# Kernel optimization log

Hardware: AMD Instinct MI355X
Metric: run time of the kernel (lower is better)

Reference implementation:

```python
import jax, jax.numpy as jnp
import numpy as np

N_NODES = 100000
F_IN = 64
F_OUT = 64
SLOPE = 0.2


def setup_inputs() -> dict:
    key = jax.random.key(0)
    k1, k2, k3, k4 = jax.random.split(key, 4)
    input_matrix = jax.random.normal(k1, (N_NODES, F_IN), dtype=jnp.float32)
    edge_index = jax.random.randint(k2, (2, 1600000), 0, N_NODES, dtype=jnp.int64)
    # xavier-uniform-style params
    lim_w = float(np.sqrt(6.0 / (F_IN + F_OUT)))
    W = jax.random.uniform(k3, (F_IN, F_OUT), minval=-lim_w, maxval=lim_w, dtype=jnp.float32)
    lim_a = float(np.sqrt(6.0 / (2 * F_OUT + 1)))
    a = jax.random.uniform(k4, (2 * F_OUT,), minval=-lim_a, maxval=lim_a, dtype=jnp.float32)
    return {"input_matrix": input_matrix, "edge_index": edge_index, "W": W, "a": a}


def reference(input_matrix, edge_index, W, a):
    N = input_matrix.shape[0]
    # add self edges
    loops = jnp.arange(N, dtype=edge_index.dtype)
    src = jnp.concatenate([edge_index[0], loops])  # [E+N]
    dst = jnp.concatenate([edge_index[1], loops])  # [E+N]

    h = input_matrix @ W                      # [N, F_out]
    F = h.shape[1]
    h_src = h[src]                            # [E+N, F_out] gather
    h_dst = h[dst]                            # [E+N, F_out] gather
    # cat([h_src, h_dst], 1) @ a == h_src @ a[:F] + h_dst @ a[F:]
    alpha = h_src @ a[:F] + h_dst @ a[F:]     # [E+N]
    alpha = jnp.where(alpha >= 0, alpha, SLOPE * alpha)  # leaky relu
    alpha = jnp.exp(alpha)
    denom = jax.ops.segment_sum(alpha, src, num_segments=N)  # [N]
    alpha = alpha / denom[src]                # segment softmax over edges sharing src
    out = jax.ops.segment_sum(h_dst * alpha[:, None], src, num_segments=N)  # [N, F_out]
    return out
```

## Files before the change

### kernel.cpp

```cpp
#include <hip/hip_runtime.h>
#include <hip/hip_bf16.h>

#define F 64
#define SLOPE 0.2f
#define NB_SHIFT 8
#define BATCH 4096
#define SLAB 5120

typedef __attribute__((ext_vector_type(8))) short bf16x8;
typedef __attribute__((ext_vector_type(4))) float f32x4;

__device__ inline unsigned short f2bf(float f) {
    unsigned u = __float_as_uint(f);
    unsigned r = (u + 0x7FFFu + ((u >> 16) & 1u)) >> 16;
    return (unsigned short)r;
}

__global__ __launch_bounds__(256) void gat_prep(
    const float* __restrict__ W, const float* __restrict__ a,
    unsigned short* __restrict__ Wp, float* __restrict__ w1,
    float* __restrict__ w2, int* __restrict__ bucketCursor) {
    int tid = threadIdx.x;
    for (int i = tid; i < 512; i += 256) bucketCursor[i] = i * SLAB;

    if (tid < 64) {
#pragma unroll
        for (int f = 0; f < 8; ++f) {
            int cg = f >> 1, kc = f & 1;
            int col = cg * 16 + (tid & 15);
            unsigned short us[8];
#pragma unroll
            for (int j = 0; j < 8; ++j) {
                int k = kc * 32 + (tid >> 4) * 8 + j;
                us[j] = f2bf(W[k * F + col]);
            }
            uint4 pk;
            pk.x = us[0] | ((unsigned)us[1] << 16);
            pk.y = us[2] | ((unsigned)us[3] << 16);
            pk.z = us[4] | ((unsigned)us[5] << 16);
            pk.w = us[6] | ((unsigned)us[7] << 16);
            *(uint4*)&Wp[(f * 64 + tid) * 8] = pk;
        }
    } else if (tid < 128) {
        int k = tid - 64;
        float acc1 = 0.f, acc2 = 0.f;
#pragma unroll
        for (int n = 0; n < F; ++n) {
            float wv = W[k * F + n];
            acc1 = fmaf(wv, a[n], acc1);
            acc2 = fmaf(wv, a[F + n], acc2);
        }
        w1[k] = acc1;
        w2[k] = acc2;
    }
}

__global__ __launch_bounds__(512) void gat_gemm_bin(
    const float* __restrict__ X, const unsigned short* __restrict__ Wp,
    const float* __restrict__ w1, const float* __restrict__ w2,
    unsigned short* __restrict__ hb, float* __restrict__ s1,
    float* __restrict__ s2, int N,
    const int* __restrict__ src, const int* __restrict__ dst,
    int* __restrict__ bucketCursor, unsigned* __restrict__ bucketData, int E,
    int gemmBlocks) {
    __shared__ int hist[512], excl[512], gbase[512], cur[512];
    __shared__ int wsum[8];
    __shared__ int2 staged[BATCH];

    int tid = threadIdx.x;
    int lane = tid & 63, wid = tid >> 6;

    if ((int)blockIdx.x >= gemmBlocks) {
        int base = (blockIdx.x - gemmBlocks) * BATCH;
        int n = E - base;
        if (n > BATCH) n = BATCH;

        hist[tid] = 0;
        __syncthreads();

        int se[8], de[8];
#pragma unroll
        for (int j = 0; j < 8; ++j) {
            int i = base + j * 512 + tid;
            se[j] = -1;
            de[j] = 0;
            if (i < E) {
                se[j] = src[i];
                de[j] = dst[i];
                atomicAdd(&hist[se[j] >> NB_SHIFT], 1);
            }
        }
        __syncthreads();
        int v = hist[tid];
        int x = v;
#pragma unroll
        for (int off = 1; off < 64; off <<= 1) {
            int y = __shfl_up(x, off, 64);
            if (lane >= off) x += y;
        }
        if (lane == 63) wsum[wid] = x;
        __syncthreads();
        int add = 0;
        for (int w = 0; w < 8; ++w)
            if (w < wid) add += wsum[w];
        int ex = add + x - v;
        excl[tid] = ex;
        cur[tid] = ex;
        __syncthreads();
#pragma unroll
        for (int j = 0; j < 8; ++j) {
            if (se[j] >= 0) {
                int b = se[j] >> NB_SHIFT;
                int pos = atomicAdd(&cur[b], 1);
                staged[pos] = make_int2(se[j], de[j]);
            }
        }
        if (v > 0)
            gbase[tid] = atomicAdd(&bucketCursor[tid], v);
        __syncthreads();
        for (int i = tid; i < n; i += 512) {
            int2 p = staged[i];
            int b = p.x >> NB_SHIFT;
            bucketData[gbase[b] + (i - excl[b])] =
                ((unsigned)(p.x & 255) << 24) | (unsigned)p.y;
        }
        return;
    }

    int rowBase = blockIdx.x * 128 + wid * 16;
    if (rowBase >= N) return;
    int lrow = lane & 15;
    int kg = lane >> 4;
    int row = rowBase + lrow;
    int rclamp = (row < N) ? row : (N - 1);

    const float* xp = &X[(size_t)rclamp * F + kg * 8];
    float4 u0 = *(const float4*)(xp + 0);
    float4 u1 = *(const float4*)(xp + 4);
    float4 u2 = *(const float4*)(xp + 32);
    float4 u3 = *(const float4*)(xp + 36);
    float xr[16] = {u0.x, u0.y, u0.z, u0.w, u1.x, u1.y, u1.z, u1.w,
                    u2.x, u2.y, u2.z, u2.w, u3.x, u3.y, u3.z, u3.w};

    bf16x8 a0, a1;
#pragma unroll
    for (int j = 0; j < 8; ++j) {
        a0[j] = (short)f2bf(xr[j]);
        a1[j] = (short)f2bf(xr[8 + j]);
    }

    bf16x8 bf0 = *(const bf16x8*)&Wp[(0 * 64 + lane) * 8];
    bf16x8 bf1 = *(const bf16x8*)&Wp[(1 * 64 + lane) * 8];
    bf16x8 bf2 = *(const bf16x8*)&Wp[(2 * 64 + lane) * 8];
    bf16x8 bf3 = *(const bf16x8*)&Wp[(3 * 64 + lane) * 8];
    bf16x8 bf4 = *(const bf16x8*)&Wp[(4 * 64 + lane) * 8];
    bf16x8 bf5 = *(const bf16x8*)&Wp[(5 * 64 + lane) * 8];
    bf16x8 bf6 = *(const bf16x8*)&Wp[(6 * 64 + lane) * 8];
    bf16x8 bf7 = *(const bf16x8*)&Wp[(7 * 64 + lane) * 8];

    f32x4 acc0 = {0.f, 0.f, 0.f, 0.f};
    f32x4 acc1v = {0.f, 0.f, 0.f, 0.f};
    f32x4 acc2v = {0.f, 0.f, 0.f, 0.f};
    f32x4 acc3 = {0.f, 0.f, 0.f, 0.f};
    acc0 = __builtin_amdgcn_mfma_f32_16x16x32_bf16(a0, bf0, acc0, 0, 0, 0);
    acc0 = __builtin_amdgcn_mfma_f32_16x16x32_bf16(a1, bf1, acc0, 0, 0, 0);
    acc1v = __builtin_amdgcn_mfma_f32_16x16x32_bf16(a0, bf2, acc1v, 0, 0, 0);
    acc1v = __builtin_amdgcn_mfma_f32_16x16x32_bf16(a1, bf3, acc1v, 0, 0, 0);
    acc2v = __builtin_amdgcn_mfma_f32_16x16x32_bf16(a0, bf4, acc2v, 0, 0, 0);
    acc2v = __builtin_amdgcn_mfma_f32_16x16x32_bf16(a1, bf5, acc2v, 0, 0, 0);
    acc3 = __builtin_amdgcn_mfma_f32_16x16x32_bf16(a0, bf6, acc3, 0, 0, 0);
    acc3 = __builtin_amdgcn_mfma_f32_16x16x32_bf16(a1, bf7, acc3, 0, 0, 0);

#pragma unroll
    for (int r = 0; r < 4; ++r) {
        int ro = rowBase + kg * 4 + r;
        if (ro < N) {
            size_t rb = (size_t)ro * F + lrow;
            hb[rb + 0] = f2bf(acc0[r]);
            hb[rb + 16] = f2bf(acc1v[r]);
            hb[rb + 32] = f2bf(acc2v[r]);
            hb[rb + 48] = f2bf(acc3[r]);
        }
    }

    float4 wa0 = *(const float4*)&w1[kg * 8];
    float4 wa1 = *(const float4*)&w1[kg * 8 + 4];
    float4 wa2 = *(const float4*)&w1[32 + kg * 8];
    float4 wa3 = *(const float4*)&w1[32 + kg * 8 + 4];
    float4 wb0 = *(const float4*)&w2[kg * 8];
    float4 wb1 = *(const float4*)&w2[kg * 8 + 4];
    float4 wb2 = *(const float4*)&w2[32 + kg * 8];
    float4 wb3 = *(const float4*)&w2[32 + kg * 8 + 4];
    float wv1[16] = {wa0.x, wa0.y, wa0.z, wa0.w, wa1.x, wa1.y, wa1.z, wa1.w,
                     wa2.x, wa2.y, wa2.z, wa2.w, wa3.x, wa3.y, wa3.z, wa3.w};
    float wv2[16] = {wb0.x, wb0.y, wb0.z, wb0.w, wb1.x, wb1.y, wb1.z, wb1.w,
                     wb2.x, wb2.y, wb2.z, wb2.w, wb3.x, wb3.y, wb3.z, wb3.w};
    float p = 0.f, q = 0.f;
#pragma unroll
    for (int j = 0; j < 16; ++j) {
        p = fmaf(xr[j], wv1[j], p);
        q = fmaf(xr[j], wv2[j], q);
    }
    p += __shfl_xor(p, 16, 64);
    p += __shfl_xor(p, 32, 64);
    q += __shfl_xor(q, 16, 64);
    q += __shfl_xor(q, 32, 64);
    if (lane < 16 && row < N) {
        s1[row] = p;
        s2[row] = q;
    }
}

__global__ __launch_bounds__(256) void gat_bucket(
    const int* __restrict__ bucketCursor, const unsigned* __restrict__ bucketData,
    const float* __restrict__ s1, const float* __restrict__ s2,
    int* __restrict__ rowbeg, int* __restrict__ rowend,
    int2* __restrict__ sortedData, int N) {
    __shared__ int cnt[256], cur[256];
    __shared__ float s1l[256];
    __shared__ int wsum[4];
    int b = blockIdx.x;
    int tid = threadIdx.x, lane = tid & 63, wid = tid >> 6;
    int beg = b * SLAB;
    int end = bucketCursor[b];
    int node0 = b << NB_SHIFT;
    int node = node0 + tid;

    cnt[tid] = 0;
    s1l[tid] = (node < N) ? s1[node] : 0.f;
    __syncthreads();
    for (int i = beg + tid; i < end; i += 256)
        atomicAdd(&cnt[bucketData[i] >> 24], 1);
    __syncthreads();
    int v = cnt[tid];
    int x = v;
#pragma unroll
    for (int off = 1; off < 64; off <<= 1) {
        int y = __shfl_up(x, off, 64);
        if (lane >= off) x += y;
    }
    if (lane == 63) wsum[wid] = x;
    __syncthreads();
    int add = 0;
    for (int w = 0; w < 4; ++w)
        if (w < wid) add += wsum[w];
    int excl = add + x - v;
    if (node < N) {
        rowbeg[node] = beg + excl;
        rowend[node] = beg + excl + v;
    }
    cur[tid] = beg + excl;
    __syncthreads();
    for (int i = beg + tid; i < end; i += 256) {
        unsigned w = bucketData[i];
        int sloc = w >> 24;
        int d = (int)(w & 0xFFFFFFu);
        float t = s1l[sloc] + s2[d];
        t = (t >= 0.f) ? t : SLOPE * t;
        float al = expf(t);
        int pos = atomicAdd(&cur[sloc], 1);
        sortedData[pos] = make_int2(d, __float_as_int(al));
    }
}

#define EDGE_FMA(g, al, A)                                                   \
    A[0] = fmaf(al, __uint_as_float(g.x << 16), A[0]);                       \
    A[1] = fmaf(al, __uint_as_float(g.x & 0xFFFF0000u), A[1]);               \
    A[2] = fmaf(al, __uint_as_float(g.y << 16), A[2]);                       \
    A[3] = fmaf(al, __uint_as_float(g.y & 0xFFFF0000u), A[3]);               \
    A[4] = fmaf(al, __uint_as_float(g.z << 16), A[4]);                       \
    A[5] = fmaf(al, __uint_as_float(g.z & 0xFFFF0000u), A[5]);               \
    A[6] = fmaf(al, __uint_as_float(g.w << 16), A[6]);                       \
    A[7] = fmaf(al, __uint_as_float(g.w & 0xFFFF0000u), A[7]);

__global__ __launch_bounds__(256) void gat_aggregate(
    const int* __restrict__ rowbeg, const int* __restrict__ rowend,
    const int2* __restrict__ sortedData,
    const float* __restrict__ s1, const float* __restrict__ s2,
    const unsigned short* __restrict__ hb, float* __restrict__ out, int N) {
    int tid = threadIdx.x;
    int node = blockIdx.x * 32 + (tid >> 3);
    if (node >= N) return;
    const int fo = (tid & 7) * 8;

    int beg = rowbeg[node];
    int end = rowend[node];
    float as = s1[node] + s2[node];
    as = (as >= 0.f) ? as : SLOPE * as;
    as = expf(as);

    float accA[8], accB[8];
    {
        uint4 hv = *(const uint4*)&hb[(size_t)node * F + fo];
        accA[0] = as * __uint_as_float(hv.x << 16);
        accA[1] = as * __uint_as_float(hv.x & 0xFFFF0000u);
        accA[2] = as * __uint_as_float(hv.y << 16);
        accA[3] = as * __uint_as_float(hv.y & 0xFFFF0000u);
        accA[4] = as * __uint_as_float(hv.z << 16);
        accA[5] = as * __uint_as_float(hv.z & 0xFFFF0000u);
        accA[6] = as * __uint_as_float(hv.w << 16);
        accA[7] = as * __uint_as_float(hv.w & 0xFFFF0000u);
    }
#pragma unroll
    for (int i = 0; i < 8; ++i) accB[i] = 0.f;

    float dsum = as;
    int e = beg;
    for (; e + 4 <= end; e += 4) {
        int2 p0 = sortedData[e];
        int2 p1 = sortedData[e + 1];
        int2 p2 = sortedData[e + 2];
        int2 p3 = sortedData[e + 3];
        uint4 g0 = *(const uint4*)&hb[(size_t)p0.x * F + fo];
        uint4 g1 = *(const uint4*)&hb[(size_t)p1.x * F + fo];
        uint4 g2 = *(const uint4*)&hb[(size_t)p2.x * F + fo];
        uint4 g3 = *(const uint4*)&hb[(size_t)p3.x * F + fo];
        float a0 = __int_as_float(p0.y);
        float a1 = __int_as_float(p1.y);
        float a2 = __int_as_float(p2.y);
        float a3 = __int_as_float(p3.y);
        dsum += (a0 + a1) + (a2 + a3);
        EDGE_FMA(g0, a0, accA);
        EDGE_FMA(g1, a1, accB);
        EDGE_FMA(g2, a2, accA);
        EDGE_FMA(g3, a3, accB);
    }
    for (; e < end; ++e) {
        int2 p0 = sortedData[e];
        float a0 = __int_as_float(p0.y);
        dsum += a0;
        uint4 g0 = *(const uint4*)&hb[(size_t)p0.x * F + fo];
        EDGE_FMA(g0, a0, accA);
    }

    float inv = 1.0f / dsum;
    float4 r0, r1;
    r0.x = (accA[0] + accB[0]) * inv;
    r0.y = (accA[1] + accB[1]) * inv;
    r0.z = (accA[2] + accB[2]) * inv;
    r0.w = (accA[3] + accB[3]) * inv;
    r1.x = (accA[4] + accB[4]) * inv;
    r1.y = (accA[5] + accB[5]) * inv;
    r1.z = (accA[6] + accB[6]) * inv;
    r1.w = (accA[7] + accB[7]) * inv;
    *(float4*)&out[(size_t)node * F + fo] = r0;
    *(float4*)&out[(size_t)node * F + fo + 4] = r1;
}

extern "C" void kernel_launch(void* const* d_in, const int* in_sizes, int n_in,
                              void* d_out, int out_size, void* d_ws, size_t ws_size,
                              hipStream_t stream) {
    const float* X = (const float*)d_in[0];
    const int* edge = (const int*)d_in[1];
    const float* W = (const float*)d_in[2];
    const float* a = (const float*)d_in[3];

    int N = in_sizes[0] / F;
    int E = in_sizes[1] / 2;
    int NB = (N + 255) >> NB_SHIFT;

    const int* src = edge;
    const int* dst = edge + E;

    unsigned* bucketData = (unsigned*)d_ws;
    int2* sortedData = (int2*)(bucketData + (size_t)NB * SLAB);
    unsigned short* hb = (unsigned short*)(sortedData + (size_t)NB * SLAB);
    float* s1 = (float*)(hb + (size_t)N * F);
    float* s2 = s1 + N;
    int* rowbeg = (int*)(s2 + N);
    int* rowend = rowbeg + N;
    int* bucketCursor = rowend + N;
    unsigned short* Wp = (unsigned short*)(bucketCursor + 512);
    float* w1 = (float*)(Wp + 4096);
    float* w2 = w1 + 64;

    float* out = (float*)d_out;

    gat_prep<<<1, 256, 0, stream>>>(W, a, Wp, w1, w2, bucketCursor);

    int gemmBlocks = (N + 127) / 128;
    int binBlocks = (E + BATCH - 1) / BATCH;
    gat_gemm_bin<<<gemmBlocks + binBlocks, 512, 0, stream>>>(
        X, Wp, w1, w2, hb, s1, s2, N, src, dst, bucketCursor, bucketData, E,
        gemmBlocks);

    gat_bucket<<<NB, 256, 0, stream>>>(bucketCursor, bucketData, s1, s2,
                                       rowbeg, rowend, sortedData, N);

    int aggBlocks = (N + 31) / 32;
    gat_aggregate<<<aggBlocks, 256, 0, stream>>>(rowbeg, rowend, sortedData,
                                                 s1, s2, hb, out, N);
}
```

Measured before the change: 87.48 us.

## Halve scatter batch, stage bucket slab in LDS, vectorize sorted edge loads

```diff
diff --git a/kernel.cpp b/kernel.cpp
--- a/kernel.cpp
+++ b/kernel.cpp
@@ -4,7 +4,7 @@
 #define F 64
 #define SLOPE 0.2f
 #define NB_SHIFT 8
-#define BATCH 4096
+#define BATCH 2048
 #define SLAB 5120
 
 typedef __attribute__((ext_vector_type(8))) short bf16x8;
@@ -78,9 +78,9 @@
         hist[tid] = 0;
         __syncthreads();
 
-        int se[8], de[8];
-#pragma unroll
-        for (int j = 0; j < 8; ++j) {
+        int se[4], de[4];
+#pragma unroll
+        for (int j = 0; j < 4; ++j) {
             int i = base + j * 512 + tid;
             se[j] = -1;
             de[j] = 0;
@@ -108,7 +108,7 @@
         cur[tid] = ex;
         __syncthreads();
 #pragma unroll
-        for (int j = 0; j < 8; ++j) {
+        for (int j = 0; j < 4; ++j) {
             if (se[j] >= 0) {
                 int b = se[j] >> NB_SHIFT;
                 int pos = atomicAdd(&cur[b], 1);
@@ -216,6 +216,7 @@
     const float* __restrict__ s1, const float* __restrict__ s2,
     int* __restrict__ rowbeg, int* __restrict__ rowend,
     int2* __restrict__ sortedData, int N) {
+    __shared__ unsigned edl[SLAB];
     __shared__ int cnt[256], cur[256];
     __shared__ float s1l[256];
     __shared__ int wsum[4];
@@ -223,14 +224,18 @@
     int tid = threadIdx.x, lane = tid & 63, wid = tid >> 6;
     int beg = b * SLAB;
     int end = bucketCursor[b];
+    int n = end - beg;
     int node0 = b << NB_SHIFT;
     int node = node0 + tid;
 
     cnt[tid] = 0;
     s1l[tid] = (node < N) ? s1[node] : 0.f;
     __syncthreads();
-    for (int i = beg + tid; i < end; i += 256)
-        atomicAdd(&cnt[bucketData[i] >> 24], 1);
+    for (int i = tid; i < n; i += 256) {
+        unsigned w = bucketData[beg + i];
+        edl[i] = w;
+        atomicAdd(&cnt[w >> 24], 1);
+    }
     __syncthreads();
     int v = cnt[tid];
     int x = v;
@@ -251,8 +256,8 @@
     }
     cur[tid] = beg + excl;
     __syncthreads();
-    for (int i = beg + tid; i < end; i += 256) {
-        unsigned w = bucketData[i];
+    for (int i = tid; i < n; i += 256) {
+        unsigned w = edl[i];
         int sloc = w >> 24;
         int d = (int)(w & 0xFFFFFFu);
         float t = s1l[sloc] + s2[d];
@@ -306,19 +311,25 @@
 
     float dsum = as;
     int e = beg;
+    if ((e & 1) && e < end) {
+        int2 p0 = sortedData[e];
+        float a0 = __int_as_float(p0.y);
+        dsum += a0;
+        uint4 g0 = *(const uint4*)&hb[(size_t)p0.x * F + fo];
+        EDGE_FMA(g0, a0, accA);
+        ++e;
+    }
     for (; e + 4 <= end; e += 4) {
-        int2 p0 = sortedData[e];
-        int2 p1 = sortedData[e + 1];
-        int2 p2 = sortedData[e + 2];
-        int2 p3 = sortedData[e + 3];
-        uint4 g0 = *(const uint4*)&hb[(size_t)p0.x * F + fo];
-        uint4 g1 = *(const uint4*)&hb[(size_t)p1.x * F + fo];
-        uint4 g2 = *(const uint4*)&hb[(size_t)p2.x * F + fo];
-        uint4 g3 = *(const uint4*)&hb[(size_t)p3.x * F + fo];
-        float a0 = __int_as_float(p0.y);
-        float a1 = __int_as_float(p1.y);
-        float a2 = __int_as_float(p2.y);
-        float a3 = __int_as_float(p3.y);
+        int4 q0 = *(const int4*)&sortedData[e];
+        int4 q1 = *(const int4*)&sortedData[e + 2];
+        uint4 g0 = *(const uint4*)&hb[(size_t)q0.x * F + fo];
+        uint4 g1 = *(const uint4*)&hb[(size_t)q0.z * F + fo];
+        uint4 g2 = *(const uint4*)&hb[(size_t)q1.x * F + fo];
+        uint4 g3 = *(const uint4*)&hb[(size_t)q1.z * F + fo];
+        float a0 = __int_as_float(q0.y);
+        float a1 = __int_as_float(q0.w);
+        float a2 = __int_as_float(q1.y);
+        float a3 = __int_as_float(q1.w);
         dsum += (a0 + a1) + (a2 + a3);
         EDGE_FMA(g0, a0, accA);
         EDGE_FMA(g1, a1, accB);
```

Result: slower. 93.37 us (+6.7%).
